# Optimization experiments

Hardware: AMD Instinct MI355X
Metric: run time of the kernel (lower is better)

## Reference

```python
import jax, jax.numpy as jnp
import numpy as np

B, S, E = 2, 2048, 2048
N_HEAD = 16
HEAD_DIM = E // N_HEAD  # 128
MP_NUM = 4              # hardcoded in the torch forward
ROTARY_DIM = 64


def setup_inputs() -> dict:
    key = jax.random.key(0)
    k1, k2, k3 = jax.random.split(key, 3)
    return {
        "hidden_states": jax.random.normal(k1, (B, S, E), jnp.float32) * 0.02,
        "w_qkv": jax.random.normal(k2, (3 * E, E), jnp.float32) * 0.02,  # torch Linear weight [out,in]
        "w_out": jax.random.normal(k3, (E, E), jnp.float32) * 0.02,
    }


def _rotate_every_two(x):
    # (..., d) -> interleaved (-x2, x1) as in GPT-J/CodeGen
    x1 = x[..., 0::2]
    x2 = x[..., 1::2]
    return jnp.stack((-x2, x1), axis=-1).reshape(x.shape)


def reference(hidden_states, w_qkv, w_out):
    b, s, e = hidden_states.shape
    local = e // MP_NUM  # per-mp-shard channel count

    # qkv projection (no bias), then mp_num split: order is (query, value, key)
    qkv = jnp.einsum("bse,fe->bsf", hidden_states, w_qkv)  # [B,S,3E]
    qkv = qkv.reshape(b, s, MP_NUM, 3 * local)
    q = qkv[..., :local].reshape(b, s, N_HEAD, HEAD_DIM)
    v = qkv[..., local:2 * local].reshape(b, s, N_HEAD, HEAD_DIM)
    k = qkv[..., 2 * local:].reshape(b, s, N_HEAD, HEAD_DIM)

    # partial rotary (rotate-every-two) on first ROTARY_DIM channels
    inv_freq = 1.0 / (10000.0 ** (jnp.arange(0, ROTARY_DIM, 2, dtype=jnp.float32) / ROTARY_DIM))
    freqs = jnp.arange(s, dtype=jnp.float32)[:, None] * inv_freq[None, :]  # [S, R/2]
    sin = jnp.repeat(jnp.sin(freqs), 2, axis=-1)[None, :, None, :]  # [1,S,1,R]
    cos = jnp.repeat(jnp.cos(freqs), 2, axis=-1)[None, :, None, :]

    def rope(x):
        x_rot = x[..., :ROTARY_DIM]
        x_pass = x[..., ROTARY_DIM:]
        x_rot = x_rot * cos + _rotate_every_two(x_rot) * sin
        return jnp.concatenate([x_rot, x_pass], axis=-1)

    q = rope(q)
    k = rope(k)

    # [B,S,H,D] -> [B,H,S,D]
    q = q.transpose(0, 2, 1, 3)
    k = k.transpose(0, 2, 1, 3)
    v = v.transpose(0, 2, 1, 3)

    scale = jnp.sqrt(jnp.asarray(HEAD_DIM, dtype=q.dtype))
    scores = jnp.einsum("bhqd,bhkd->bhqk", q, k) / scale  # [B,H,S,S]
    causal = jnp.tril(jnp.ones((s, s), dtype=bool))
    scores = jnp.where(causal[None, None, :, :], scores, jnp.finfo(scores.dtype).min)
    attn = jax.nn.softmax(scores, axis=-1)

    out = jnp.einsum("bhqk,bhkd->bhqd", attn, v)  # [B,H,S,D]
    out = out.transpose(0, 2, 1, 3).reshape(b, s, e)  # merge heads
    return jnp.einsum("bse,fe->bsf", out, w_out)  # out_proj (no bias)
```

## Files before the change

### kernel.cpp

```cpp
#include <hip/hip_runtime.h>

typedef unsigned short u16;
typedef unsigned int u32;
typedef __attribute__((ext_vector_type(4))) float f32x4;
typedef __attribute__((ext_vector_type(8))) short s16x8;

#define DEVI static __device__ __forceinline__


#define ROPE_C (-13.287712379549449f / 32.0f)
#define QSCALE 0.12751743f

DEVI u16 f2bf(float f) {
  u32 u = __float_as_uint(f);
  return (u16)((u + 0x7FFFu + ((u >> 16) & 1u)) >> 16);
}
DEVI float bf2f(u16 h) { return __uint_as_float(((u32)h) << 16); }

DEVI void async_copy16(const u16* g, u16* l) {
  __builtin_amdgcn_global_load_lds((__attribute__((address_space(1))) void*)g,
                                   (__attribute__((address_space(3))) void*)l, 16, 0, 0);
}

__global__ __launch_bounds__(256) void cast3_kernel(
    const float* __restrict__ s0, u16* __restrict__ d0, int n0,
    const float* __restrict__ s1, u16* __restrict__ d1, int n1,
    const float* __restrict__ s2, u16* __restrict__ d2, int n2) {
  int i = blockIdx.x * 256 + threadIdx.x;
  const float* s;
  u16* d;
  if (i < n0) {
    s = s0; d = d0;
  } else if (i < n0 + n1) {
    s = s1; d = d1; i -= n0;
  } else if (i < n0 + n1 + n2) {
    s = s2; d = d2; i -= n0 + n1;
  } else {
    return;
  }
  const float4 v = ((const float4*)s)[i];
  ushort4 o;
  o.x = f2bf(v.x); o.y = f2bf(v.y); o.z = f2bf(v.z); o.w = f2bf(v.w);
  ((ushort4*)d)[i] = o;
}

template <int EPI>
__global__ __launch_bounds__(256, 3) void gemm_bt_kernel(
    const u16* __restrict__ A, const u16* __restrict__ Bm, int K, int N,
    float* __restrict__ C, u16* __restrict__ qo, u16* __restrict__ ko, u16* __restrict__ vo) {
  __shared__ __attribute__((aligned(16))) u16 As[3][128 * 32];
  __shared__ __attribute__((aligned(16))) u16 Bs[3][128 * 32];
  const int tid = threadIdx.x;
  const int w = tid >> 6, lane = tid & 63;
  const int quad = lane >> 4, l16 = lane & 15;
  const int wrow = (w >> 1) * 64, wcol = (w & 1) * 64;
  const long tileM = (long)blockIdx.y * 128;
  const long tileN = (long)blockIdx.x * 128;

  f32x4 acc[4][4];
#pragma unroll
  for (int i = 0; i < 4; ++i)
#pragma unroll
    for (int j = 0; j < 4; ++j) acc[i][j] = f32x4{0.f, 0.f, 0.f, 0.f};

  const u16* aptr[2];
  const u16* bptr[2];
  int ldso[2];
#pragma unroll
  for (int c = 0; c < 2; ++c) {
    const int r0 = (w * 2 + c) * 16;
    const int row = r0 + (lane >> 2);
    const int colsw = (((lane & 3) ^ ((row >> 1) & 3)) << 3);
    aptr[c] = A + (tileM + row) * (long)K + colsw;
    bptr[c] = Bm + (tileN + row) * (long)K + colsw;
    ldso[c] = r0 * 32;
  }

  auto stage = [&](int k0, int buf) {
#pragma unroll
    for (int c = 0; c < 2; ++c) {
      async_copy16(aptr[c] + k0, &As[buf][ldso[c]]);
      async_copy16(bptr[c] + k0, &Bs[buf][ldso[c]]);
    }
  };

  stage(0, 0);
  stage(32, 1);

  const int psw = (quad ^ ((l16 >> 1) & 3)) << 3;

  int bt = 0;
  for (int k0 = 0; k0 < K; k0 += 32) {
    if (k0 + 32 < K)
      __builtin_amdgcn_s_waitcnt(0x0f74);
    else
      __builtin_amdgcn_s_waitcnt(0x0f70);
    __builtin_amdgcn_s_barrier();
    if (k0 + 64 < K) stage(k0 + 64, bt == 0 ? 2 : bt - 1);

    s16x8 af[4], bfr[4];
#pragma unroll
    for (int i = 0; i < 4; ++i)
      af[i] = *(const s16x8*)(&As[bt][(wrow + i * 16 + l16) * 32 + psw]);
#pragma unroll
    for (int j = 0; j < 4; ++j)
      bfr[j] = *(const s16x8*)(&Bs[bt][(wcol + j * 16 + l16) * 32 + psw]);
#pragma unroll
    for (int i = 0; i < 4; ++i)
#pragma unroll
      for (int j = 0; j < 4; ++j)
        acc[i][j] = __builtin_amdgcn_mfma_f32_16x16x32_bf16(af[i], bfr[j], acc[i][j], 0, 0, 0);
    bt = bt == 2 ? 0 : bt + 1;
  }

  const int b = (int)(tileM >> 11);
#pragma unroll
  for (int i = 0; i < 4; ++i) {
#pragma unroll
    for (int j = 0; j < 4; ++j) {
      const int rowb = (int)((tileM + wrow + i * 16 + quad * 4) & 2047);
      if (EPI == 0) {
#pragma unroll
        for (int r = 0; r < 4; ++r) {
          const long row = tileM + wrow + i * 16 + quad * 4 + r;
          C[row * N + tileN + wcol + j * 16 + l16] = acc[i][j][r];
        }
      } else {
        const long col0 = tileN + wcol + j * 16;
        const int mp = (int)(col0 / 1536);
        const int cc0 = (int)(col0 - (long)mp * 1536);
        const int part = cc0 >> 9;
        const int idx0 = cc0 & 511;
        const int head = mp * 4 + (idx0 >> 7);
        const int dim0 = idx0 & 127;
        const int dim = dim0 + l16;
        const long bh = (long)(b * 16 + head);
        if (part == 1) {
#pragma unroll
          for (int r = 0; r < 4; ++r)
            vo[(bh * 128 + dim) * 2048 + rowb + r] = f2bf(acc[i][j][r]);
        } else {
          float y[4];
          if (part == 2 && dim0 < 64) {
            const int jj = dim >> 1;
            const float inv = exp2f((float)jj * ROPE_C);
#pragma unroll
            for (int r = 0; r < 4; ++r) {
              const float v = acc[i][j][r];
              const float pv = __shfl_xor(v, 1, 64);
              const float ang = (float)(rowb + r) * inv;
              const float sn = sinf(ang), cs = cosf(ang);
              y[r] = (l16 & 1) ? (v * cs + pv * sn) : (v * cs - pv * sn);
            }
          } else {
#pragma unroll
            for (int r = 0; r < 4; ++r) y[r] = acc[i][j][r];
          }
          u16* dst = (part == 0) ? qo : ko;
#pragma unroll
          for (int r = 0; r < 4; ++r)
            dst[(bh * 2048 + rowb + r) * 128 + dim] = f2bf(y[r]);
        }
      }
    }
  }
}

__global__ __launch_bounds__(256, 4) void attn_kernel(
    const u16* __restrict__ q, const u16* __restrict__ k,
    const u16* __restrict__ vT, u16* __restrict__ out) {
  __shared__ __attribute__((aligned(16))) u16 Ks[2][32 * 128];
  __shared__ __attribute__((aligned(16))) u16 Vs[2][128 * 32];
  __shared__ __attribute__((aligned(16))) u16 Ps[4][16 * 40];
  const int tid = threadIdx.x;
  const int w = tid >> 6, lane = tid & 63;
  const int quad = lane >> 4, l16 = lane & 15;
  const int qt = 31 - (blockIdx.x >> 5);
  const int bh = blockIdx.x & 31;
  const int qbase = qt * 64 + w * 16;

  const u16* qp = q + ((long)bh * 2048 + qbase) * 128;
  const u16* kp = k + (long)bh * 2048 * 128;
  const u16* vp = vT + (long)bh * 128 * 2048;

  const float spos = (float)(qbase + l16);
  s16x8 qf[4];
#pragma unroll
  for (int c = 0; c < 4; ++c) {
    const s16x8 raw = *(const s16x8*)(qp + l16 * 128 + c * 32 + quad * 8);
    s16x8 ov;
    if (c < 2) {
#pragma unroll
      for (int m = 0; m < 4; ++m) {
        const int jj = c * 16 + quad * 4 + m;
        const float inv = exp2f((float)jj * ROPE_C);
        const float ang = spos * inv;
        const float sn = sinf(ang), cs = cosf(ang);
        const float x0 = bf2f((u16)raw[2 * m]), x1 = bf2f((u16)raw[2 * m + 1]);
        ov[2 * m] = (short)f2bf((x0 * cs - x1 * sn) * QSCALE);
        ov[2 * m + 1] = (short)f2bf((x1 * cs + x0 * sn) * QSCALE);
      }
    } else {
#pragma unroll
      for (int e = 0; e < 8; ++e) ov[e] = (short)f2bf(bf2f((u16)raw[e]) * QSCALE);
    }
    qf[c] = ov;
  }

  f32x4 acc[8];
#pragma unroll
  for (int d = 0; d < 8; ++d) acc[d] = f32x4{0.f, 0.f, 0.f, 0.f};
  float mrun[4], lrun[4];
#pragma unroll
  for (int r = 0; r < 4; ++r) { mrun[r] = -1e30f; lrun[r] = 0.f; }

  auto stage = [&](int k0, int buf) {
    const int ko = lane >> 4, cl = lane & 15;
#pragma unroll
    for (int i = 0; i < 2; ++i) {
      const int keyt = w * 8 + i * 4;
      const int key = keyt + ko;
      async_copy16(kp + (long)(k0 + key) * 128 + ((cl ^ (key & 15)) << 3),
                   &Ks[buf][keyt * 128]);
    }
    const int ld = lane >> 2, c4 = lane & 3;
#pragma unroll
    for (int i = 0; i < 2; ++i) {
      const int db = w * 32 + i * 16;
      const int d = db + ld;
      async_copy16(vp + (long)d * 2048 + k0 + ((c4 ^ ((d >> 1) & 3)) << 3),
                   &Vs[buf][db * 32]);
    }
  };

  stage(0, 0);

  const int nt = 2 * qt + 2;
  for (int t = 0; t < nt; ++t) {
    const int k0 = t * 32;
    const u16* Ksc = Ks[t & 1];
    const u16* Vsc = Vs[t & 1];
    __builtin_amdgcn_s_waitcnt(0x0f70);
    __syncthreads();
    if (t + 1 < nt) stage(k0 + 32, (t + 1) & 1);

    f32x4 sc[2];
#pragma unroll
    for (int g = 0; g < 2; ++g) {
      sc[g] = f32x4{0.f, 0.f, 0.f, 0.f};
#pragma unroll
      for (int c = 0; c < 4; ++c) {
        const s16x8 kf = *(const s16x8*)(
            &Ksc[(g * 16 + l16) * 128 + ((((c << 2) + quad) ^ l16) << 3)]);
        sc[g] = __builtin_amdgcn_mfma_f32_16x16x32_bf16(qf[c], kf, sc[g], 0, 0, 0);
      }
    }
    if (k0 + 31 > qbase) {
#pragma unroll
      for (int g = 0; g < 2; ++g) {
        const int col = k0 + g * 16 + l16;
#pragma unroll
        for (int r = 0; r < 4; ++r)
          if (col > qbase + quad * 4 + r) sc[g][r] = -1e30f;
      }
    }
    float p[2][4], alpha[4];
#pragma unroll
    for (int r = 0; r < 4; ++r) {
      float mx = fmaxf(sc[0][r], sc[1][r]);
#pragma unroll
      for (int off = 1; off < 16; off <<= 1) mx = fmaxf(mx, __shfl_xor(mx, off, 64));
      const float mnew = fmaxf(mrun[r], mx);
      alpha[r] = exp2f(mrun[r] - mnew);
      mrun[r] = mnew;
      float sm = 0.f;
#pragma unroll
      for (int g = 0; g < 2; ++g) { p[g][r] = exp2f(sc[g][r] - mnew); sm += p[g][r]; }
#pragma unroll
      for (int off = 1; off < 16; off <<= 1) sm += __shfl_xor(sm, off, 64);
      lrun[r] = lrun[r] * alpha[r] + sm;
    }
#pragma unroll
    for (int d = 0; d < 8; ++d)
#pragma unroll
      for (int r = 0; r < 4; ++r) acc[d][r] *= alpha[r];
#pragma unroll
    for (int r = 0; r < 4; ++r)
#pragma unroll
      for (int g = 0; g < 2; ++g)
        Ps[w][(quad * 4 + r) * 40 + g * 16 + l16] = f2bf(p[g][r]);
    __builtin_amdgcn_s_waitcnt(0xc07f);
    const s16x8 pf = *(const s16x8*)(&Ps[w][l16 * 40 + quad * 8]);
#pragma unroll
    for (int dd = 0; dd < 8; ++dd) {
      const s16x8 vf = *(const s16x8*)(
          &Vsc[(dd * 16 + l16) * 32 + ((quad ^ ((l16 >> 1) & 3)) << 3)]);
      acc[dd] = __builtin_amdgcn_mfma_f32_16x16x32_bf16(pf, vf, acc[dd], 0, 0, 0);
    }
  }

  const int b = bh >> 4, h = bh & 15;
  u16* op = out + ((long)b * 2048 + qbase) * 2048 + h * 128;
#pragma unroll
  for (int d = 0; d < 8; ++d)
#pragma unroll
    for (int r = 0; r < 4; ++r) {
      const float v = acc[d][r] / lrun[r];
      op[(long)(quad * 4 + r) * 2048 + d * 16 + l16] = f2bf(v);
    }
}

extern "C" void kernel_launch(void* const* d_in, const int* in_sizes, int n_in,
                              void* d_out, int out_size, void* d_ws, size_t ws_size,
                              hipStream_t stream) {
  const float* hidden = (const float*)d_in[0];
  const float* w_qkv = (const float*)d_in[1];
  const float* w_out = (const float*)d_in[2];
  float* out = (float*)d_out;
  char* ws = (char*)d_ws;

  u16* hid_b  = (u16*)(ws + (size_t)0);
  u16* wqkv_b = (u16*)(ws + (size_t)16777216);
  u16* wout_b = (u16*)(ws + (size_t)41943040);
  u16* qb     = (u16*)(ws + (size_t)50331648);
  u16* kb     = (u16*)(ws + (size_t)67108864);
  u16* vb     = (u16*)(ws + (size_t)83886080);
  u16* ao     = (u16*)(ws + (size_t)100663296);

  cast3_kernel<<<24576, 256, 0, stream>>>(hidden, hid_b, 2097152,
                                          w_qkv, wqkv_b, 3145728,
                                          w_out, wout_b, 1048576);

  gemm_bt_kernel<1><<<dim3(48, 32), 256, 0, stream>>>(hid_b, wqkv_b, 2048, 6144,
                                                      nullptr, qb, kb, vb);
  attn_kernel<<<1024, 256, 0, stream>>>(qb, kb, vb, ao);
  gemm_bt_kernel<0><<<dim3(16, 32), 256, 0, stream>>>(ao, wout_b, 2048, 2048,
                                                      out, nullptr, nullptr, nullptr);
}
```

Baseline: 461.4 us.

## Transpose attention MFMAs so softmax rows live per lane and drop LDS P staging

Swaps the MFMA operand order so the score tile is key-major, which puts each query row in one lane column. Row max and sum then reduce with two cross-lane shuffles instead of four 16-wide reductions, and the running max and sum become single scalars. P is repacked into the PV MFMA operand with register shuffles instead of a round trip through LDS. The output is written as vectorized 4-wide stores with one reciprocal, and the RoPE sin/cos calls switch to the fast intrinsics. The fast intrinsics trade some precision, which could matter at large angles.

```diff
diff --git a/kernel.cpp b/kernel.cpp
--- a/kernel.cpp
+++ b/kernel.cpp
@@ -4,6 +4,7 @@
 typedef unsigned int u32;
 typedef __attribute__((ext_vector_type(4))) float f32x4;
 typedef __attribute__((ext_vector_type(8))) short s16x8;
+typedef __attribute__((ext_vector_type(4))) unsigned int u32x4;
 
 #define DEVI static __device__ __forceinline__
 
@@ -149,7 +150,7 @@
               const float v = acc[i][j][r];
               const float pv = __shfl_xor(v, 1, 64);
               const float ang = (float)(rowb + r) * inv;
-              const float sn = sinf(ang), cs = cosf(ang);
+              const float sn = __sinf(ang), cs = __cosf(ang);
               y[r] = (l16 & 1) ? (v * cs + pv * sn) : (v * cs - pv * sn);
             }
           } else {
@@ -171,7 +172,6 @@
     const u16* __restrict__ vT, u16* __restrict__ out) {
   __shared__ __attribute__((aligned(16))) u16 Ks[2][32 * 128];
   __shared__ __attribute__((aligned(16))) u16 Vs[2][128 * 32];
-  __shared__ __attribute__((aligned(16))) u16 Ps[4][16 * 40];
   const int tid = threadIdx.x;
   const int w = tid >> 6, lane = tid & 63;
   const int quad = lane >> 4, l16 = lane & 15;
@@ -195,7 +195,7 @@
         const int jj = c * 16 + quad * 4 + m;
         const float inv = exp2f((float)jj * ROPE_C);
         const float ang = spos * inv;
-        const float sn = sinf(ang), cs = cosf(ang);
+        const float sn = __sinf(ang), cs = __cosf(ang);
         const float x0 = bf2f((u16)raw[2 * m]), x1 = bf2f((u16)raw[2 * m + 1]);
         ov[2 * m] = (short)f2bf((x0 * cs - x1 * sn) * QSCALE);
         ov[2 * m + 1] = (short)f2bf((x1 * cs + x0 * sn) * QSCALE);
@@ -210,9 +210,7 @@
   f32x4 acc[8];
 #pragma unroll
   for (int d = 0; d < 8; ++d) acc[d] = f32x4{0.f, 0.f, 0.f, 0.f};
-  float mrun[4], lrun[4];
-#pragma unroll
-  for (int r = 0; r < 4; ++r) { mrun[r] = -1e30f; lrun[r] = 0.f; }
+  float mrun = -1e30f, lrun = 0.f;
 
   auto stage = [&](int k0, int buf) {
     const int ko = lane >> 4, cl = lane & 15;
@@ -252,62 +250,80 @@
       for (int c = 0; c < 4; ++c) {
         const s16x8 kf = *(const s16x8*)(
             &Ksc[(g * 16 + l16) * 128 + ((((c << 2) + quad) ^ l16) << 3)]);
-        sc[g] = __builtin_amdgcn_mfma_f32_16x16x32_bf16(qf[c], kf, sc[g], 0, 0, 0);
+        sc[g] = __builtin_amdgcn_mfma_f32_16x16x32_bf16(kf, qf[c], sc[g], 0, 0, 0);
       }
     }
     if (k0 + 31 > qbase) {
+      const int qrow = qbase + l16;
 #pragma unroll
       for (int g = 0; g < 2; ++g) {
-        const int col = k0 + g * 16 + l16;
+        const int keyb = k0 + g * 16 + quad * 4;
 #pragma unroll
         for (int r = 0; r < 4; ++r)
-          if (col > qbase + quad * 4 + r) sc[g][r] = -1e30f;
+          if (keyb + r > qrow) sc[g][r] = -1e30f;
       }
     }
-    float p[2][4], alpha[4];
-#pragma unroll
-    for (int r = 0; r < 4; ++r) {
-      float mx = fmaxf(sc[0][r], sc[1][r]);
-#pragma unroll
-      for (int off = 1; off < 16; off <<= 1) mx = fmaxf(mx, __shfl_xor(mx, off, 64));
-      const float mnew = fmaxf(mrun[r], mx);
-      alpha[r] = exp2f(mrun[r] - mnew);
-      mrun[r] = mnew;
-      float sm = 0.f;
-#pragma unroll
-      for (int g = 0; g < 2; ++g) { p[g][r] = exp2f(sc[g][r] - mnew); sm += p[g][r]; }
-#pragma unroll
-      for (int off = 1; off < 16; off <<= 1) sm += __shfl_xor(sm, off, 64);
-      lrun[r] = lrun[r] * alpha[r] + sm;
-    }
+    float mx = fmaxf(fmaxf(fmaxf(sc[0][0], sc[0][1]), fmaxf(sc[0][2], sc[0][3])),
+                     fmaxf(fmaxf(sc[1][0], sc[1][1]), fmaxf(sc[1][2], sc[1][3])));
+    mx = fmaxf(mx, __shfl_xor(mx, 16, 64));
+    mx = fmaxf(mx, __shfl_xor(mx, 32, 64));
+    const float mnew = fmaxf(mrun, mx);
+    const float alpha = exp2f(mrun - mnew);
+    mrun = mnew;
+    float p[2][4];
+    float sm = 0.f;
+#pragma unroll
+    for (int g = 0; g < 2; ++g)
+#pragma unroll
+      for (int r = 0; r < 4; ++r) { p[g][r] = exp2f(sc[g][r] - mnew); sm += p[g][r]; }
+    sm += __shfl_xor(sm, 16, 64);
+    sm += __shfl_xor(sm, 32, 64);
+    lrun = lrun * alpha + sm;
 #pragma unroll
     for (int d = 0; d < 8; ++d)
 #pragma unroll
-      for (int r = 0; r < 4; ++r) acc[d][r] *= alpha[r];
-#pragma unroll
-    for (int r = 0; r < 4; ++r)
-#pragma unroll
-      for (int g = 0; g < 2; ++g)
-        Ps[w][(quad * 4 + r) * 40 + g * 16 + l16] = f2bf(p[g][r]);
-    __builtin_amdgcn_s_waitcnt(0xc07f);
-    const s16x8 pf = *(const s16x8*)(&Ps[w][l16 * 40 + quad * 8]);
+      for (int r = 0; r < 4; ++r) acc[d][r] *= alpha;
+
+    u32 pk[2][2];
+#pragma unroll
+    for (int g = 0; g < 2; ++g) {
+      pk[g][0] = (u32)f2bf(p[g][0]) | ((u32)f2bf(p[g][1]) << 16);
+      pk[g][1] = (u32)f2bf(p[g][2]) | ((u32)f2bf(p[g][3]) << 16);
+    }
+    const int la = ((quad & 1) << 5) + l16;
+    const int lb = la + 16;
+    const u32 a0 = (u32)__shfl((int)pk[0][0], la, 64);
+    const u32 a1 = (u32)__shfl((int)pk[0][1], la, 64);
+    const u32 a2 = (u32)__shfl((int)pk[0][0], lb, 64);
+    const u32 a3 = (u32)__shfl((int)pk[0][1], lb, 64);
+    const u32 b0 = (u32)__shfl((int)pk[1][0], la, 64);
+    const u32 b1 = (u32)__shfl((int)pk[1][1], la, 64);
+    const u32 b2 = (u32)__shfl((int)pk[1][0], lb, 64);
+    const u32 b3 = (u32)__shfl((int)pk[1][1], lb, 64);
+    const bool hi = quad >= 2;
+    const u32x4 pw = {hi ? b0 : a0, hi ? b1 : a1, hi ? b2 : a2, hi ? b3 : a3};
+    const s16x8 pf = __builtin_bit_cast(s16x8, pw);
+
 #pragma unroll
     for (int dd = 0; dd < 8; ++dd) {
       const s16x8 vf = *(const s16x8*)(
           &Vsc[(dd * 16 + l16) * 32 + ((quad ^ ((l16 >> 1) & 3)) << 3)]);
-      acc[dd] = __builtin_amdgcn_mfma_f32_16x16x32_bf16(pf, vf, acc[dd], 0, 0, 0);
+      acc[dd] = __builtin_amdgcn_mfma_f32_16x16x32_bf16(vf, pf, acc[dd], 0, 0, 0);
     }
   }
 
   const int b = bh >> 4, h = bh & 15;
-  u16* op = out + ((long)b * 2048 + qbase) * 2048 + h * 128;
-#pragma unroll
-  for (int d = 0; d < 8; ++d)
-#pragma unroll
-    for (int r = 0; r < 4; ++r) {
-      const float v = acc[d][r] / lrun[r];
-      op[(long)(quad * 4 + r) * 2048 + d * 16 + l16] = f2bf(v);
-    }
+  u16* op = out + ((long)b * 2048 + qbase + l16) * 2048 + h * 128;
+  const float inv_l = 1.0f / lrun;
+#pragma unroll
+  for (int dd = 0; dd < 8; ++dd) {
+    ushort4 o4;
+    o4.x = f2bf(acc[dd][0] * inv_l);
+    o4.y = f2bf(acc[dd][1] * inv_l);
+    o4.z = f2bf(acc[dd][2] * inv_l);
+    o4.w = f2bf(acc[dd][3] * inv_l);
+    *(ushort4*)(op + dd * 16 + quad * 4) = o4;
+  }
 }
 
 extern "C" void kernel_launch(void* const* d_in, const int* in_sizes, int n_in,
```

New measurement: 382.3 us. 1.21x faster.
